# Optimization experiments

Measured on AMD Instinct MI355X. Metric: run time of the kernel, lower is better.

The kernel has to match this reference:

```python
import jax, jax.numpy as jnp
import numpy as np

B, S, H = 8, 2048, 1024
NEG = -1e10


def setup_inputs() -> dict:
    key = jax.random.key(0)
    ks = jax.random.split(key, 8)
    scale = 1.0 / np.sqrt(H)
    return {
        "x": jax.random.normal(ks[0], (B, S, H), dtype=jnp.float32),
        "pad_mask": jax.random.randint(ks[1], (B, S), 0, 2, dtype=jnp.int32),
        "Wq": jax.random.uniform(ks[2], (H, H), jnp.float32, -scale, scale),
        "bq": jax.random.uniform(ks[3], (H,), jnp.float32, -scale, scale),
        "Wk": jax.random.uniform(ks[4], (H, H), jnp.float32, -scale, scale),
        "bk": jax.random.uniform(ks[5], (H,), jnp.float32, -scale, scale),
        "Wv": jax.random.uniform(ks[6], (H, H), jnp.float32, -scale, scale),
        "bv": jax.random.uniform(ks[7], (H,), jnp.float32, -scale, scale),
    }


def reference(x, pad_mask, Wq, bq, Wk, bk, Wv, bv):
    # Linear projections (torch Linear: x @ W.T + b)
    q = x @ Wq.T + bq  # [B,S,H]
    k = x @ Wk.T + bk
    v = x @ Wv.T + bv
    weight = jnp.einsum("bid,bjd->bij", q, k)  # [B,S,S]
    seq = x.shape[1]
    # causal mask (strictly upper triangular) + padding mask over key positions
    causal = jnp.triu(jnp.ones((seq, seq), dtype=jnp.float32), k=1)  # [S,S]
    pad = pad_mask.astype(jnp.float32)[:, None, :]  # [B,1,S] -> key axis
    mask = (causal[None, :, :] + pad) > 0  # [B,S,S]
    # torch code fills BEFORE scaling; replicate exactly
    weight = jnp.where(mask, NEG, weight)
    score = jax.nn.softmax(weight / jnp.sqrt(jnp.float32(weight.shape[-1] * 0 + x.shape[-1])), axis=-1)
    return jnp.einsum("bij,bjd->bid", score, v)
```

## Files before the change

### kernel.cpp

```cpp
#include <hip/hip_runtime.h>

typedef __attribute__((ext_vector_type(8))) short short8;
typedef __attribute__((ext_vector_type(4))) short short4v;
typedef __attribute__((ext_vector_type(4))) float float4v;

typedef const __attribute__((address_space(1))) unsigned int* gptr_t;
typedef __attribute__((address_space(3))) unsigned int* lptr_t;

__device__ __forceinline__ unsigned short f2bf(float f) {
  unsigned u = __float_as_uint(f);
  u += 0x7FFFu + ((u >> 16) & 1u);
  return (unsigned short)(u >> 16);
}
__device__ __forceinline__ float bf2f(unsigned short h) {
  return __uint_as_float(((unsigned)h) << 16);
}

__global__ __launch_bounds__(256) void cvtW_kernel(const float* __restrict__ Wq,
                                                   const float* __restrict__ Wk,
                                                   const float* __restrict__ Wv,
                                                   unsigned short* __restrict__ wb) {
  int blk = blockIdx.x;
  int r = blk >> 10;
  const float* src = (r == 0) ? Wq : ((r == 1) ? Wk : Wv);
  int t = threadIdx.x;
  int i = (blk & 1023) * 256 + t;
  float4v v = ((const float4v*)src)[i];
  short4v o;
  o[0] = (short)f2bf(v[0]);
  o[1] = (short)f2bf(v[1]);
  o[2] = (short)f2bf(v[2]);
  o[3] = (short)f2bf(v[3]);
  ((short4v*)(wb + (size_t)r * 1048576u))[i] = o;
}

__global__ __launch_bounds__(256) void compact_kernel(const int* __restrict__ pad,
                                                      int* __restrict__ jmap,
                                                      int* __restrict__ cntb,
                                                      float* __restrict__ mean_x) {
  int b = blockIdx.x;
  const int* prow = pad + b * 2048;
  int t = threadIdx.x;
  float4v z = {0.f, 0.f, 0.f, 0.f};
  ((float4v*)(mean_x + b * 1024))[t] = z;
  int base = t * 8;
  int ind[8], incl[8];
  int s = 0;
#pragma unroll
  for (int e = 0; e < 8; ++e) {
    ind[e] = (prow[base + e] == 0);
    s += ind[e];
    incl[e] = s;
  }
  int lane = t & 63, wv = t >> 6;
  int v = s;
#pragma unroll
  for (int off = 1; off < 64; off <<= 1) {
    int u = __shfl_up(v, off);
    if (lane >= off) v += u;
  }
  __shared__ int wsum[4];
  if (lane == 63) wsum[wv] = v;
  __syncthreads();
  int wbase = 0;
  for (int w = 0; w < wv; ++w) wbase += wsum[w];
  int excl_base = wbase + v - s;
#pragma unroll
  for (int e = 0; e < 8; ++e) {
    int cnt_i = excl_base + incl[e];
    cntb[b * 2048 + base + e] = cnt_i;
    if (ind[e]) jmap[b * 2048 + cnt_i - 1] = base + e;
  }
}

__global__ __launch_bounds__(256) void prep_kernel(const float* __restrict__ x,
                                                   const int* __restrict__ pad,
                                                   const int* __restrict__ cntb,
                                                   unsigned short* __restrict__ xb,
                                                   unsigned short* __restrict__ xc) {
  int i = blockIdx.x, b = blockIdx.y;
  int idx = b * 2048 + i;
  int t = threadIdx.x;
  float4v v = ((const float4v*)(x + (size_t)idx * 1024))[t];
  short4v o;
  o[0] = (short)f2bf(v[0]);
  o[1] = (short)f2bf(v[1]);
  o[2] = (short)f2bf(v[2]);
  o[3] = (short)f2bf(v[3]);
  ((short4v*)(xb + (size_t)idx * 1024))[t] = o;
  if (pad[idx] == 0) {
    int jc = cntb[idx] - 1;
    ((short4v*)(xc + ((size_t)(b * 2048 + jc)) * 1024))[t] = o;
  }
  int Nc = cntb[b * 2048 + 2047];
  if (i >= Nc && i < ((Nc + 127) & ~127)) {
    short4v z = {0, 0, 0, 0};
    ((short4v*)(xc + ((size_t)(b * 2048 + i)) * 1024))[t] = z;
  }
}

__global__ __launch_bounds__(256) void meanx_kernel(const unsigned short* __restrict__ xb,
                                                    float* __restrict__ mean_x) {
  int iblk = blockIdx.x, b = blockIdx.y;
  int t = threadIdx.x;
  const unsigned short* base = xb + ((size_t)b * 2048 + (size_t)iblk * 64) * 1024 + t * 4;
  float s0 = 0.f, s1 = 0.f, s2 = 0.f, s3 = 0.f;
  for (int r = 0; r < 64; ++r) {
    short4v v = *(const short4v*)(base + (size_t)r * 1024);
    s0 += bf2f(((const unsigned short*)&v)[0]);
    s1 += bf2f(((const unsigned short*)&v)[1]);
    s2 += bf2f(((const unsigned short*)&v)[2]);
    s3 += bf2f(((const unsigned short*)&v)[3]);
  }
  float* mp = mean_x + b * 1024 + t * 4;
  atomicAdd(mp + 0, s0);
  atomicAdd(mp + 1, s1);
  atomicAdd(mp + 2, s2);
  atomicAdd(mp + 3, s3);
}

template <int MODE>
__global__ __launch_bounds__(256, 4) void gemm_bt_kernel(
    const unsigned short* __restrict__ A, const unsigned short* __restrict__ A2,
    const unsigned short* __restrict__ B,
    const float* __restrict__ b1, const float* __restrict__ b2, const float* __restrict__ b3,
    void* __restrict__ C, unsigned short* __restrict__ C2, unsigned short* __restrict__ C3,
    const int* __restrict__ cnt,
    int K, int lda, int ldb, int ldc, size_t sA, size_t sB, size_t sC) {
  int bx = blockIdx.x, by = blockIdx.y, bz = blockIdx.z;
  const unsigned short* Aptr = A;
  if (MODE == 0) {
    int wg = by * 24 + bx;
    int s = (wg & 7) * 384 + (wg >> 3);
    bx = s % 24;
    by = s / 24;
    int r = bx >> 3;
    if (r > 0) {
      int b = by >> 4;
      if (((by & 15) << 7) >= cnt[(b << 11) + 2047]) return;
      Aptr = A2;
    }
  }
  if (MODE == 1) {
    int wg = by * 16 + bx;
    int s = (wg & 7) * 32 + (wg >> 3);
    bx = s & 15;
    by = s >> 4;
  }
  if (MODE == 2) {
    int wg = by * 8 + bx;
    int s = (wg & 7) * 16 + (wg >> 3);
    bx = s & 7;
    by = s >> 3;
  }
  int Kend = K;
  if (MODE == 1) {
    int tc = cnt[(bz << 11) + (by * 128 + 127)];
    if (bx * 128 >= tc) return;
  }
  if (MODE == 2) {
    int tc = cnt[(bz << 11) + (by * 128 + 127)];
    Kend = (tc + 63) & ~63;
  }

  __shared__ __align__(16) char lds[32768];
  char* ldsA = lds;
  char* ldsB = lds + 16384;

  int tid = threadIdx.x;
  int wave = tid >> 6, lane = tid & 63;
  int lm = lane & 15, g = lane >> 4;
  int wm = wave >> 1, wn = wave & 1;
  int swl = (lm & 7) << 4;

  float4v acc[4][4];
#pragma unroll
  for (int i = 0; i < 4; ++i)
#pragma unroll
    for (int j = 0; j < 4; ++j) {
      float4v z = {0.f, 0.f, 0.f, 0.f};
      acc[i][j] = z;
    }

  const char* Abase = (const char*)(Aptr + sA * (size_t)bz + (size_t)(by * 128) * (size_t)lda);
  const char* Bbase = (const char*)(B + sB * (size_t)bz + (size_t)(bx * 128) * (size_t)ldb);
  size_t strideA = (size_t)lda * 2u;
  size_t strideB = (size_t)ldb * 2u;

  int Lbase = wave * 1024 + lane * 16;

  for (int kt = 0; kt < Kend; kt += 64) {
#pragma unroll
    for (int c = 0; c < 4; ++c) {
      int L = c * 4096 + Lbase;
      int row = L >> 7;
      int lb = (L & 127) ^ ((row & 7) << 4);
      const char* ga = Abase + (size_t)row * strideA + (size_t)(kt * 2) + lb;
      __builtin_amdgcn_global_load_lds((gptr_t)(const void*)ga,
                                       (lptr_t)(void*)(ldsA + c * 4096 + wave * 1024), 16, 0, 0);
      const char* gb = Bbase + (size_t)row * strideB + (size_t)(kt * 2) + lb;
      __builtin_amdgcn_global_load_lds((gptr_t)(const void*)gb,
                                       (lptr_t)(void*)(ldsB + c * 4096 + wave * 1024), 16, 0, 0);
    }
    __syncthreads();

#pragma unroll
    for (int k0 = 0; k0 < 64; k0 += 32) {
      short8 af[4], bfv[4];
      int b0 = (k0 * 2 + 16 * g) ^ swl;
#pragma unroll
      for (int mi = 0; mi < 4; ++mi) {
        const char* p = ldsA + (wm * 64 + mi * 16 + lm) * 128;
        af[mi] = *(const short8*)(p + b0);
      }
#pragma unroll
      for (int ni = 0; ni < 4; ++ni) {
        const char* p = ldsB + (wn * 64 + ni * 16 + lm) * 128;
        bfv[ni] = *(const short8*)(p + b0);
      }
#pragma unroll
      for (int mi = 0; mi < 4; ++mi)
#pragma unroll
        for (int ni = 0; ni < 4; ++ni)
          acc[mi][ni] =
              __builtin_amdgcn_mfma_f32_16x16x32_bf16(af[mi], bfv[ni], acc[mi][ni], 0, 0, 0);
    }
    __syncthreads();
  }

  int mb = by * 128 + wm * 64 + g * 4;
  int nb = bx * 128 + wn * 64 + lm;
#pragma unroll
  for (int mi = 0; mi < 4; ++mi) {
#pragma unroll
    for (int ni = 0; ni < 4; ++ni) {
      int n = nb + ni * 16;
      float bias = 0.0f;
      if (MODE == 0) {
        int nn = n & 1023;
        int r = n >> 10;
        bias = (r == 0) ? b1[nn] : ((r == 1) ? b2[nn] : b3[nn]);
      }
#pragma unroll
      for (int r4 = 0; r4 < 4; ++r4) {
        int m = mb + mi * 16 + r4;
        float v = acc[mi][ni][r4] + bias;
        if (MODE == 0) {
          int nn = n & 1023;
          int r = n >> 10;
          if (r == 0) {
            ((unsigned short*)C)[(size_t)m * 1024u + nn] = f2bf(v);
          } else if (r == 1) {
            C3[(size_t)m * 1024u + nn] = f2bf(v);
          } else {
            size_t idx = ((size_t)(m >> 11) << 21) + ((size_t)nn << 11) + (size_t)(m & 2047);
            C2[idx] = f2bf(v);
          }
        } else if (MODE == 1) {
          ((unsigned short*)C)[sC * (size_t)bz + (size_t)m * (size_t)ldc + n] = f2bf(v);
        } else {
          ((float*)C)[sC * (size_t)bz + (size_t)m * (size_t)ldc + n] = v;
        }
      }
    }
  }
}

__global__ __launch_bounds__(256) void softmax_kernel(unsigned short* __restrict__ sp,
                                                      const int* __restrict__ cntb) {
  int i = blockIdx.x, b = blockIdx.y;
  int cnt_i = cntb[b * 2048 + i];
  int tcnt = cntb[b * 2048 + (i | 127)];
  int W = (tcnt + 63) & ~63;
  unsigned short* row = sp + ((size_t)b * 2048 + (size_t)i) * 2048;
  int tid = threadIdx.x;
  int j0 = tid * 8;
  bool active = (j0 < W);

  float t[8];
  if (active) {
    short8 sv = *(const short8*)(row + j0);
#pragma unroll
    for (int e = 0; e < 8; ++e) {
      int jc = j0 + e;
      bool msk = (jc >= cnt_i);
      float raw = bf2f(((const unsigned short*)&sv)[e]);
      t[e] = (msk ? -1e10f : raw) * 0.03125f;
    }
  } else {
#pragma unroll
    for (int e = 0; e < 8; ++e) t[e] = -1e10f * 0.03125f;
  }

  float m = t[0];
#pragma unroll
  for (int e = 1; e < 8; ++e) m = fmaxf(m, t[e]);
#pragma unroll
  for (int o = 32; o > 0; o >>= 1) m = fmaxf(m, __shfl_xor(m, o));
  __shared__ float redm[4], reds[4];
  int wv = tid >> 6, ln = tid & 63;
  if (ln == 0) redm[wv] = m;
  __syncthreads();
  m = fmaxf(fmaxf(redm[0], redm[1]), fmaxf(redm[2], redm[3]));

  float p[8];
  float s = 0.f;
#pragma unroll
  for (int e = 0; e < 8; ++e) {
    p[e] = __expf(t[e] - m);
    s += p[e];
  }
#pragma unroll
  for (int o = 32; o > 0; o >>= 1) s += __shfl_xor(s, o);
  if (ln == 0) reds[wv] = s;
  __syncthreads();
  s = reds[0] + reds[1] + reds[2] + reds[3];
  float inv = 1.0f / s;

  if (active) {
    short8 ov;
#pragma unroll
    for (int e = 0; e < 8; ++e) ((unsigned short*)&ov)[e] = (short)f2bf(p[e] * inv);
    *(short8*)(row + j0) = ov;
  }
}

__global__ __launch_bounds__(256) void fixup_kernel(const int* __restrict__ cntb,
                                                    const float* __restrict__ mean_x,
                                                    const unsigned short* __restrict__ wv,
                                                    const float* __restrict__ bv,
                                                    float* __restrict__ out) {
  int b = blockIdx.x, dblk = blockIdx.y;
  if (cntb[b * 2048] != 0) return;
  int d = dblk * 256 + threadIdx.x;
  const unsigned short* wrow = wv + (size_t)d * 1024;
  const float* mx = mean_x + b * 1024;
  float s = 0.f;
  for (int h = 0; h < 1024; h += 8) {
    short8 w = *(const short8*)(wrow + h);
#pragma unroll
    for (int e = 0; e < 8; ++e) s += mx[h + e] * bf2f(((const unsigned short*)&w)[e]);
  }
  float val = s * (1.0f / 2048.0f) + bv[d];
  for (int i = 0; i < 2048; ++i) {
    if (cntb[b * 2048 + i] != 0) break;
    out[((size_t)b * 2048 + (size_t)i) * 1024 + d] = val;
  }
}

extern "C" void kernel_launch(void* const* d_in, const int* in_sizes, int n_in,
                              void* d_out, int out_size, void* d_ws, size_t ws_size,
                              hipStream_t stream) {
  const float* x = (const float*)d_in[0];
  const int* pad = (const int*)d_in[1];
  const float* Wq = (const float*)d_in[2];
  const float* bq = (const float*)d_in[3];
  const float* Wk = (const float*)d_in[4];
  const float* bk = (const float*)d_in[5];
  const float* Wv = (const float*)d_in[6];
  const float* bv = (const float*)d_in[7];
  float* out = (float*)d_out;

  char* ws = (char*)d_ws;
  unsigned short* xb  = (unsigned short*)(ws + 0);
  unsigned short* xc  = (unsigned short*)(ws + 33554432);
  unsigned short* wb  = (unsigned short*)(ws + 67108864);
  int*   jmap    = (int*)(ws + 73400320);
  int*   cntb    = (int*)(ws + 73465856);
  float* mean_x  = (float*)(ws + 73531392);
  unsigned short* qb  = (unsigned short*)(ws + 75497472);
  unsigned short* vtc = (unsigned short*)(ws + 109051904);
  unsigned short* sp  = (unsigned short*)(ws + 142606336);
  unsigned short* kcb = (unsigned short*)(ws + 209715200);

  compact_kernel<<<8, 256, 0, stream>>>(pad, jmap, cntb, mean_x);

  cvtW_kernel<<<3072, 256, 0, stream>>>(Wq, Wk, Wv, wb);
  dim3 gp(2048, 8);
  prep_kernel<<<gp, 256, 0, stream>>>(x, pad, cntb, xb, xc);
  dim3 gmx(32, 8);
  meanx_kernel<<<gmx, 256, 0, stream>>>(xb, mean_x);

  dim3 g1(24, 128, 1);
  gemm_bt_kernel<0><<<g1, 256, 0, stream>>>(xb, xc, wb, bq, bk, bv, qb, vtc, kcb, cntb,
                                            1024, 1024, 1024, 1024, 0, 0, 0);

  dim3 g4(16, 16, 8);
  gemm_bt_kernel<1><<<g4, 256, 0, stream>>>(qb, nullptr, kcb, nullptr, nullptr, nullptr,
                                            sp, nullptr, nullptr, cntb,
                                            1024, 1024, 1024, 2048, 2097152, 2097152, 4194304);

  dim3 g5(2048, 8);
  softmax_kernel<<<g5, 256, 0, stream>>>(sp, cntb);

  dim3 g6(8, 16, 8);
  gemm_bt_kernel<2><<<g6, 256, 0, stream>>>(sp, nullptr, vtc, nullptr, nullptr, nullptr,
                                            out, nullptr, nullptr, cntb,
                                            2048, 2048, 2048, 1024, 4194304, 2097152, 2097152);

  dim3 g3(8, 4);
  fixup_kernel<<<g3, 256, 0, stream>>>(cntb, mean_x, wb + 2097152, bv, out);
}
```

Before: 270.3 us.

## Replace projection GEMM with 256x256-tile double-buffered kernel

```diff
diff --git a/kernel.cpp b/kernel.cpp
--- a/kernel.cpp
+++ b/kernel.cpp
@@ -93,7 +93,7 @@
     ((short4v*)(xc + ((size_t)(b * 2048 + jc)) * 1024))[t] = o;
   }
   int Nc = cntb[b * 2048 + 2047];
-  if (i >= Nc && i < ((Nc + 127) & ~127)) {
+  if (i >= Nc && i < ((Nc + 255) & ~255)) {
     short4v z = {0, 0, 0, 0};
     ((short4v*)(xc + ((size_t)(b * 2048 + i)) * 1024))[t] = z;
   }
@@ -119,28 +119,141 @@
   atomicAdd(mp + 3, s3);
 }
 
+__global__ __launch_bounds__(512, 2) void proj256_kernel(
+    const unsigned short* __restrict__ xb, const unsigned short* __restrict__ xc,
+    const unsigned short* __restrict__ wbw,
+    const float* __restrict__ b1, const float* __restrict__ b2, const float* __restrict__ b3,
+    unsigned short* __restrict__ qb, unsigned short* __restrict__ vtc,
+    unsigned short* __restrict__ kcb, const int* __restrict__ cnt) {
+  int bx = blockIdx.x, by = blockIdx.y;
+  {
+    int wg = by * 12 + bx;
+    int s = (wg & 7) * 96 + (wg >> 3);
+    bx = s % 12;
+    by = s / 12;
+  }
+  int reg = bx >> 2;
+  const unsigned short* Aptr = xb;
+  if (reg > 0) {
+    int b = by >> 3;
+    if (((by & 7) << 8) >= cnt[(b << 11) + 2047]) return;
+    Aptr = xc;
+  }
+
+  __shared__ __align__(16) char lds[131072];
+
+  int tid = threadIdx.x;
+  int wave = tid >> 6, lane = tid & 63;
+  int lm = lane & 15, g = lane >> 4;
+  int wm = wave >> 2, wn = wave & 3;
+  int swl = (lm & 7) << 4;
+
+  float4v acc[8][4];
+#pragma unroll
+  for (int i = 0; i < 8; ++i)
+#pragma unroll
+    for (int j = 0; j < 4; ++j) {
+      float4v z = {0.f, 0.f, 0.f, 0.f};
+      acc[i][j] = z;
+    }
+
+  const char* Abase = (const char*)Aptr + (size_t)(by * 256) * 2048u;
+  const char* Bbase = (const char*)wbw + (size_t)(bx * 256) * 2048u;
+
+  const char* aSrc[4];
+  const char* bSrc[4];
+  int ldsOff[4];
+#pragma unroll
+  for (int rr = 0; rr < 4; ++rr) {
+    int L = rr * 8192 + tid * 16;
+    int h = L >> 14;
+    int Lh = L & 16383;
+    int rp = Lh >> 7;
+    int un = (Lh & 127) ^ ((rp & 7) << 4);
+    int grow = h * 128 + rp;
+    aSrc[rr] = Abase + (size_t)grow * 2048u + un;
+    bSrc[rr] = Bbase + (size_t)grow * 2048u + un;
+    ldsOff[rr] = L;
+  }
+
+  auto STAGE = [&](int t) {
+    char* slot = lds + (t & 1) * 65536;
+    int kb = t * 128;
+#pragma unroll
+    for (int rr = 0; rr < 4; ++rr) {
+      __builtin_amdgcn_global_load_lds((gptr_t)(const void*)(aSrc[rr] + kb),
+                                       (lptr_t)(void*)(slot + ldsOff[rr]), 16, 0, 0);
+      __builtin_amdgcn_global_load_lds((gptr_t)(const void*)(bSrc[rr] + kb),
+                                       (lptr_t)(void*)(slot + 32768 + ldsOff[rr]), 16, 0, 0);
+    }
+  };
+
+  const int nt = 16;
+  STAGE(0);
+  STAGE(1);
+
+  for (int t = 0; t < nt; ++t) {
+    if (t + 1 < nt)
+      asm volatile("s_waitcnt vmcnt(8)" ::: "memory");
+    else
+      asm volatile("s_waitcnt vmcnt(0)" ::: "memory");
+    asm volatile("s_barrier" ::: "memory");
+
+    const char* As = lds + (t & 1) * 65536 + wm * 16384;
+    const char* Bs = lds + (t & 1) * 65536 + 32768 + wn * 8192;
+#pragma unroll
+    for (int ks = 0; ks < 2; ++ks) {
+      int b0 = (ks * 64 + g * 16) ^ swl;
+      short8 af[8], bf8[4];
+#pragma unroll
+      for (int fr = 0; fr < 8; ++fr)
+        af[fr] = *(const short8*)(As + (fr * 16 + lm) * 128 + b0);
+#pragma unroll
+      for (int fc = 0; fc < 4; ++fc)
+        bf8[fc] = *(const short8*)(Bs + (fc * 16 + lm) * 128 + b0);
+#pragma unroll
+      for (int fr = 0; fr < 8; ++fr)
+#pragma unroll
+        for (int fc = 0; fc < 4; ++fc)
+          acc[fr][fc] =
+              __builtin_amdgcn_mfma_f32_16x16x32_bf16(af[fr], bf8[fc], acc[fr][fc], 0, 0, 0);
+    }
+    asm volatile("s_barrier" ::: "memory");
+    if (t + 2 < nt) STAGE(t + 2);
+  }
+
+  const float* bp = (reg == 0) ? b1 : ((reg == 1) ? b2 : b3);
+  int b = by >> 3;
+#pragma unroll
+  for (int fc = 0; fc < 4; ++fc) {
+    int nloc = (bx & 3) * 256 + wn * 64 + fc * 16 + lm;
+    float bias = bp[nloc];
+#pragma unroll
+    for (int fr = 0; fr < 8; ++fr) {
+#pragma unroll
+      for (int r4 = 0; r4 < 4; ++r4) {
+        int mrow = wm * 128 + fr * 16 + g * 4 + r4;
+        float v = acc[fr][fc][r4] + bias;
+        if (reg == 0) {
+          qb[(size_t)(by * 256 + mrow) * 1024u + nloc] = f2bf(v);
+        } else if (reg == 1) {
+          int mr = (by & 7) * 256 + mrow;
+          kcb[(size_t)b * 2097152u + (size_t)mr * 1024u + nloc] = f2bf(v);
+        } else {
+          int mr = (by & 7) * 256 + mrow;
+          vtc[((size_t)b << 21) + ((size_t)nloc << 11) + (size_t)mr] = f2bf(v);
+        }
+      }
+    }
+  }
+}
+
 template <int MODE>
 __global__ __launch_bounds__(256, 4) void gemm_bt_kernel(
-    const unsigned short* __restrict__ A, const unsigned short* __restrict__ A2,
-    const unsigned short* __restrict__ B,
-    const float* __restrict__ b1, const float* __restrict__ b2, const float* __restrict__ b3,
-    void* __restrict__ C, unsigned short* __restrict__ C2, unsigned short* __restrict__ C3,
-    const int* __restrict__ cnt,
+    const unsigned short* __restrict__ A, const unsigned short* __restrict__ B,
+    void* __restrict__ C, const int* __restrict__ cnt,
     int K, int lda, int ldb, int ldc, size_t sA, size_t sB, size_t sC) {
   int bx = blockIdx.x, by = blockIdx.y, bz = blockIdx.z;
-  const unsigned short* Aptr = A;
-  if (MODE == 0) {
-    int wg = by * 24 + bx;
-    int s = (wg & 7) * 384 + (wg >> 3);
-    bx = s % 24;
-    by = s / 24;
-    int r = bx >> 3;
-    if (r > 0) {
-      int b = by >> 4;
-      if (((by & 15) << 7) >= cnt[(b << 11) + 2047]) return;
-      Aptr = A2;
-    }
-  }
   if (MODE == 1) {
     int wg = by * 16 + bx;
     int s = (wg & 7) * 32 + (wg >> 3);
@@ -182,7 +295,7 @@
       acc[i][j] = z;
     }
 
-  const char* Abase = (const char*)(Aptr + sA * (size_t)bz + (size_t)(by * 128) * (size_t)lda);
+  const char* Abase = (const char*)(A + sA * (size_t)bz + (size_t)(by * 128) * (size_t)lda);
   const char* Bbase = (const char*)(B + sB * (size_t)bz + (size_t)(bx * 128) * (size_t)ldb);
   size_t strideA = (size_t)lda * 2u;
   size_t strideB = (size_t)ldb * 2u;
@@ -235,28 +348,11 @@
 #pragma unroll
     for (int ni = 0; ni < 4; ++ni) {
       int n = nb + ni * 16;
-      float bias = 0.0f;
-      if (MODE == 0) {
-        int nn = n & 1023;
-        int r = n >> 10;
-        bias = (r == 0) ? b1[nn] : ((r == 1) ? b2[nn] : b3[nn]);
-      }
 #pragma unroll
       for (int r4 = 0; r4 < 4; ++r4) {
         int m = mb + mi * 16 + r4;
-        float v = acc[mi][ni][r4] + bias;
-        if (MODE == 0) {
-          int nn = n & 1023;
-          int r = n >> 10;
-          if (r == 0) {
-            ((unsigned short*)C)[(size_t)m * 1024u + nn] = f2bf(v);
-          } else if (r == 1) {
-            C3[(size_t)m * 1024u + nn] = f2bf(v);
-          } else {
-            size_t idx = ((size_t)(m >> 11) << 21) + ((size_t)nn << 11) + (size_t)(m & 2047);
-            C2[idx] = f2bf(v);
-          }
-        } else if (MODE == 1) {
+        float v = acc[mi][ni][r4];
+        if (MODE == 1) {
           ((unsigned short*)C)[sC * (size_t)bz + (size_t)m * (size_t)ldc + n] = f2bf(v);
         } else {
           ((float*)C)[sC * (size_t)bz + (size_t)m * (size_t)ldc + n] = v;
@@ -381,22 +477,21 @@
   dim3 gmx(32, 8);
   meanx_kernel<<<gmx, 256, 0, stream>>>(xb, mean_x);
 
-  dim3 g1(24, 128, 1);
-  gemm_bt_kernel<0><<<g1, 256, 0, stream>>>(xb, xc, wb, bq, bk, bv, qb, vtc, kcb, cntb,
-                                            1024, 1024, 1024, 1024, 0, 0, 0);
+  dim3 g1(12, 64, 1);
+  proj256_kernel<<<g1, 512, 0, stream>>>(xb, xc, wb, bq, bk, bv, qb, vtc, kcb, cntb);
 
   dim3 g4(16, 16, 8);
-  gemm_bt_kernel<1><<<g4, 256, 0, stream>>>(qb, nullptr, kcb, nullptr, nullptr, nullptr,
-                                            sp, nullptr, nullptr, cntb,
-                                            1024, 1024, 1024, 2048, 2097152, 2097152, 4194304);
+  gemm_bt_kernel<1><<<g4, 256, 0, stream>>>(qb, kcb, sp, cntb,
+                                            1024, 1024, 1024, 2048,
+                                            2097152, 2097152, 4194304);
 
   dim3 g5(2048, 8);
   softmax_kernel<<<g5, 256, 0, stream>>>(sp, cntb);
 
   dim3 g6(8, 16, 8);
-  gemm_bt_kernel<2><<<g6, 256, 0, stream>>>(sp, nullptr, vtc, nullptr, nullptr, nullptr,
-                                            out, nullptr, nullptr, cntb,
-                                            2048, 2048, 2048, 1024, 4194304, 2097152, 2097152);
+  gemm_bt_kernel<2><<<g6, 256, 0, stream>>>(sp, vtc, out, cntb,
+                                            2048, 2048, 2048, 1024,
+                                            4194304, 2097152, 2097152);
 
   dim3 g3(8, 4);
   fixup_kernel<<<g3, 256, 0, stream>>>(cntb, mean_x, wb + 2097152, bv, out);
```

Measured after the change: 289.4 us. +7.1%, slower.
